# Kernel optimization log

Measured on AMD Instinct MI355X. Metric: run time of the kernel, lower is better.

The kernel has to match this reference:

```python
import jax, jax.numpy as jnp
import numpy as np

BN_EPS = 1e-5

def _sage_conv(x, src, dst, Wl, bl, Wr):
    # mean aggregation of neighbor messages: agg[v] = mean_{u->v} x[u]
    n = x.shape[0]
    s = jax.ops.segment_sum(x[src], dst, num_segments=n)            # [N, d]
    cnt = jax.ops.segment_sum(jnp.ones_like(dst, dtype=x.dtype), dst, num_segments=n)
    agg = s / jnp.maximum(cnt, 1.0)[:, None]
    return agg @ Wl + bl + x @ Wr                                   # lin_l(agg) + lin_r(x)

def _bn(x, g, b):
    mu = jnp.mean(x, axis=0)
    var = jnp.var(x, axis=0)
    return (x - mu) * jax.lax.rsqrt(var + BN_EPS) * g + b

def setup_inputs() -> dict:
    key = jax.random.key(0)
    ks = jax.random.split(key, 8)
    N, E, D, H, C = 100000, 1600000, 128, 128, 47
    sc = 1.0 / np.sqrt(D)
    return {
        "x": jax.random.normal(ks[0], (N, D), jnp.float32),
        "edge_index": jax.random.randint(ks[1], (2, E), 0, N, jnp.int64),
        "Wl0": jax.random.normal(ks[2], (D, H), jnp.float32) * sc,
        "bl0": jnp.zeros((H,), jnp.float32),
        "Wr0": jax.random.normal(ks[3], (D, H), jnp.float32) * sc,
        "g0": jnp.ones((H,), jnp.float32),
        "be0": jnp.zeros((H,), jnp.float32),
        "Wl1": jax.random.normal(ks[4], (H, H), jnp.float32) * sc,
        "bl1": jnp.zeros((H,), jnp.float32),
        "Wr1": jax.random.normal(ks[5], (H, H), jnp.float32) * sc,
        "g1": jnp.ones((H,), jnp.float32),
        "be1": jnp.zeros((H,), jnp.float32),
        "Wl2": jax.random.normal(ks[6], (H, C), jnp.float32) * sc,
        "bl2": jnp.zeros((C,), jnp.float32),
        "Wr2": jax.random.normal(ks[7], (H, C), jnp.float32) * sc,
    }

def reference(x, edge_index, Wl0, bl0, Wr0, g0, be0, Wl1, bl1, Wr1, g1, be1, Wl2, bl2, Wr2):
    src, dst = edge_index[0], edge_index[1]
    h = _sage_conv(x, src, dst, Wl0, bl0, Wr0)
    h = jax.nn.relu(_bn(h, g0, be0))
    h = _sage_conv(h, src, dst, Wl1, bl1, Wr1)
    h = jax.nn.relu(_bn(h, g1, be1))
    h = _sage_conv(h, src, dst, Wl2, bl2, Wr2)
    return jax.nn.log_softmax(h, axis=-1)
```

## Files before the change

### kernel.cpp

```cpp
#include <hip/hip_runtime.h>
#include <hip/hip_fp8.h>
#include <stdint.h>

#define AS1 __attribute__((address_space(1)))
#define AS3 __attribute__((address_space(3)))

typedef __bf16 bf16;
typedef __bf16 bf16x2 __attribute__((ext_vector_type(2)));
typedef __bf16 bf16x4v __attribute__((ext_vector_type(4)));
typedef __bf16 bf16x8 __attribute__((ext_vector_type(8)));
typedef float f32x4 __attribute__((ext_vector_type(4)));
typedef float f32x2 __attribute__((ext_vector_type(2)));
typedef __hip_fp8_e4m3 fp8;

#define BN_EPS 1e-5f
#define BKT_SHIFT 8
#define BKT_NODES 256
#define TILE_E 2048
#define NCOPY 16

__global__ void k_setup(const float* __restrict__ x, bf16* __restrict__ x_bf,
                        unsigned char* __restrict__ x8, int n4,
                        const int* __restrict__ ei, int* __restrict__ btot, int E, int nbkt,
                        const float* __restrict__ Wl0, const float* __restrict__ Wr0,
                        const float* __restrict__ Wl1, const float* __restrict__ Wr1,
                        const float* __restrict__ Wl2, const float* __restrict__ Wr2,
                        bf16* __restrict__ Bt0, bf16* __restrict__ Bt1, bf16* __restrict__ Bt2) {
    __shared__ int hist[512];
    const int tid = threadIdx.x;
    int g = blockIdx.x * 256 + tid;
    if (g < n4) {
        float4 v = ((const float4*)x)[g];
        bf16x4v o; o[0] = (bf16)v.x; o[1] = (bf16)v.y; o[2] = (bf16)v.z; o[3] = (bf16)v.w;
        ((bf16x4v*)x_bf)[g] = o;
        uchar4 o8;
        o8.x = fp8(v.x).__x; o8.y = fp8(v.y).__x; o8.z = fp8(v.z).__x; o8.w = fp8(v.w).__x;
        ((uchar4*)x8)[g] = o8;
    }
    if (blockIdx.x < 128) {
        int idx = g;
        int c = idx >> 8, k = idx & 255;
        float v0 = (k < 128) ? Wl0[k * 128 + c] : Wr0[(k - 128) * 128 + c];
        Bt0[c * 256 + k] = (bf16)v0;
        float v1 = (k < 128) ? Wl1[k * 128 + c] : Wr1[(k - 128) * 128 + c];
        Bt1[c * 256 + k] = (bf16)v1;
        if (k < 128) {
            float v2 = 0.f;
            if (c < 47)      v2 = Wl2[k * 47 + c];
            else if (c < 94) v2 = Wr2[k * 47 + (c - 47)];
            Bt2[c * 128 + k] = (bf16)v2;
        }
    }
    int nbinb = (E + 4095) / 4096;
    if (blockIdx.x < nbinb) {
        hist[tid] = 0; hist[tid + 256] = 0;
        __syncthreads();
        const int e0 = blockIdx.x * 4096;
        #pragma unroll
        for (int k = 0; k < 4; ++k) {
            int i4 = (e0 >> 2) + k * 256 + tid;
            if (i4 * 4 + 3 < E) {
                int4 d4 = ((const int4*)(ei + E))[i4];
                atomicAdd(&hist[d4.x >> BKT_SHIFT], 1);
                atomicAdd(&hist[d4.y >> BKT_SHIFT], 1);
                atomicAdd(&hist[d4.z >> BKT_SHIFT], 1);
                atomicAdd(&hist[d4.w >> BKT_SHIFT], 1);
            } else {
                for (int e = i4 * 4; e < min(E, i4 * 4 + 4); ++e)
                    atomicAdd(&hist[ei[E + e] >> BKT_SHIFT], 1);
            }
        }
        __syncthreads();
        for (int b = tid; b < nbkt; b += 256)
            if (hist[b]) atomicAdd(&btot[b], hist[b]);
    }
}

__device__ __forceinline__ void scan_btot(const int* __restrict__ btot, int nbkt,
                                          int* sb, int* wsum) {
    const int tid = threadIdx.x, lane = tid & 63, wid = tid >> 6;
    int a = (tid < nbkt) ? btot[tid] : 0;
    int b2 = (tid + 256 < nbkt) ? btot[tid + 256] : 0;
    int ia = a, ib = b2;
    #pragma unroll
    for (int d = 1; d < 64; d <<= 1) {
        int t1 = __shfl_up(ia, d, 64);
        int t2 = __shfl_up(ib, d, 64);
        if (lane >= d) { ia += t1; ib += t2; }
    }
    if (lane == 63) { wsum[wid] = ia; wsum[4 + wid] = ib; }
    __syncthreads();
    if (tid == 0) {
        int c = 0;
        #pragma unroll
        for (int i = 0; i < 8; ++i) { int t = wsum[i]; wsum[i] = c; c += t; }
    }
    __syncthreads();
    sb[tid] = ia - a + wsum[wid];
    sb[tid + 256] = ib - b2 + wsum[4 + wid];
    if (tid == 255) sb[512] = ib + wsum[7];
    __syncthreads();
}

__global__ __launch_bounds__(256) void k_bin(const int* __restrict__ ei,
                                             const int* __restrict__ btot,
                                             int* __restrict__ bfill,
                                             uint32_t* __restrict__ pair_buf,
                                             int E, int nbkt) {
    __shared__ int hist[512], gbase[512], hcur[512];
    __shared__ int sb[513], wsum[8];
    const int tid = threadIdx.x;
    const int e0 = blockIdx.x * TILE_E;
    hist[tid] = 0; hist[tid + 256] = 0;
    scan_btot(btot, nbkt, sb, wsum);

    int dreg[TILE_E / 256];
    #pragma unroll
    for (int k = 0; k < TILE_E / 256; ++k) {
        int e = e0 + k * 256 + tid;
        int d = (e < E) ? ei[E + e] : -1;
        dreg[k] = d;
        if (d >= 0) atomicAdd(&hist[d >> BKT_SHIFT], 1);
    }
    __syncthreads();

    for (int b = tid; b < nbkt; b += 256) {
        int h = hist[b];
        int g = (h > 0) ? atomicAdd(&bfill[b], h) : 0;
        gbase[b] = sb[b] + g;
        hcur[b] = 0;
    }
    __syncthreads();

    #pragma unroll
    for (int k = 0; k < TILE_E / 256; ++k) {
        int d = dreg[k];
        if (d >= 0) {
            int e = e0 + k * 256 + tid;
            int s = ei[e];
            int b = d >> BKT_SHIFT;
            int r = atomicAdd(&hcur[b], 1);
            pair_buf[(size_t)gbase[b] + r] =
                ((uint32_t)s << BKT_SHIFT) | (uint32_t)(d & (BKT_NODES - 1));
        }
    }
}

__global__ __launch_bounds__(256) void k_fill2(const uint32_t* __restrict__ pair_buf,
                                               const int* __restrict__ btot,
                                               int* __restrict__ row_ptr,
                                               float* __restrict__ inv_deg,
                                               int* __restrict__ col_idx,
                                               int n, int E, int nbkt) {
    __shared__ int hist[256], excl[256], hcur[256], wsum4[4];
    __shared__ int sb[513], wsum[8];
    const int b = blockIdx.x;
    const int tid = threadIdx.x, lane = tid & 63, wid = tid >> 6;
    const int n0 = b << BKT_SHIFT;
    hist[tid] = 0; hcur[tid] = 0;
    scan_btot(btot, nbkt, sb, wsum);
    const int s = sb[b], e = sb[b + 1];
    for (int i = s + tid; i < e; i += 256)
        atomicAdd(&hist[pair_buf[i] & (BKT_NODES - 1)], 1);
    __syncthreads();
    int v = hist[tid];
    int incl = v;
    #pragma unroll
    for (int d = 1; d < 64; d <<= 1) {
        int t = __shfl_up(incl, d, 64);
        if (lane >= d) incl += t;
    }
    if (lane == 63) wsum4[wid] = incl;
    __syncthreads();
    if (tid == 0) {
        int c = 0;
        #pragma unroll
        for (int i = 0; i < 4; ++i) { int t = wsum4[i]; wsum4[i] = c; c += t; }
    }
    __syncthreads();
    int ex = incl - v + wsum4[wid];
    excl[tid] = ex;
    int node = n0 + tid;
    if (node < n) {
        row_ptr[node] = s + ex;
        inv_deg[node] = 1.0f / (float)(v > 1 ? v : 1);
    }
    if (b == (int)gridDim.x - 1 && tid == 0) row_ptr[n] = E;
    __syncthreads();
    for (int i = s + tid; i < e; i += 256) {
        uint32_t pk = pair_buf[i];
        int dl = pk & (BKT_NODES - 1);
        int r = atomicAdd(&hcur[dl], 1);
        col_idx[s + excl[dl] + r] = (int)(pk >> BKT_SHIFT);
    }
}

#define ACC4(u) { f32x2 pl_ = __builtin_amdgcn_cvt_pk_f32_fp8(u, false); \
                  f32x2 ph_ = __builtin_amdgcn_cvt_pk_f32_fp8(u, true);  \
                  a0 += pl_[0]; a1 += pl_[1]; a2 += ph_[0]; a3 += ph_[1]; }
__global__ void k_aggregate(const unsigned char* __restrict__ src8, bf16* __restrict__ dst,
                            const int* __restrict__ row_ptr, const int* __restrict__ col_idx,
                            const float* __restrict__ inv_deg, int n) {
    const int lane = threadIdx.x & 63;
    const int half = lane >> 5;
    const int sl = lane & 31;
    const int node = blockIdx.x * 8 + ((threadIdx.x >> 6) << 1) + half;
    const bool valid = node < n;
    const int nn = valid ? node : 0;
    const int re0 = row_ptr[nn];
    const int re1 = valid ? row_ptr[nn + 1] : re0;
    const float inv = inv_deg[nn];
    const uint32_t l4 = (uint32_t)(sl << 2);
    float a0 = 0.f, a1 = 0.f, a2 = 0.f, a3 = 0.f;
    int e = re0;
    for (; e < re1 && (e & 3); ++e) {
        uint32_t u = *(const uint32_t*)(src8 + (((uint32_t)col_idx[e] << 7) + l4));
        ACC4(u)
    }
    for (; e + 16 <= re1; e += 16) {
        int4 i0 = *(const int4*)(col_idx + e);
        int4 i1 = *(const int4*)(col_idx + e + 4);
        int4 i2 = *(const int4*)(col_idx + e + 8);
        int4 i3 = *(const int4*)(col_idx + e + 12);
        uint32_t u0  = *(const uint32_t*)(src8 + (((uint32_t)i0.x << 7) + l4));
        uint32_t u1  = *(const uint32_t*)(src8 + (((uint32_t)i0.y << 7) + l4));
        uint32_t u2  = *(const uint32_t*)(src8 + (((uint32_t)i0.z << 7) + l4));
        uint32_t u3  = *(const uint32_t*)(src8 + (((uint32_t)i0.w << 7) + l4));
        uint32_t u4  = *(const uint32_t*)(src8 + (((uint32_t)i1.x << 7) + l4));
        uint32_t u5  = *(const uint32_t*)(src8 + (((uint32_t)i1.y << 7) + l4));
        uint32_t u6  = *(const uint32_t*)(src8 + (((uint32_t)i1.z << 7) + l4));
        uint32_t u7  = *(const uint32_t*)(src8 + (((uint32_t)i1.w << 7) + l4));
        uint32_t u8  = *(const uint32_t*)(src8 + (((uint32_t)i2.x << 7) + l4));
        uint32_t u9  = *(const uint32_t*)(src8 + (((uint32_t)i2.y << 7) + l4));
        uint32_t u10 = *(const uint32_t*)(src8 + (((uint32_t)i2.z << 7) + l4));
        uint32_t u11 = *(const uint32_t*)(src8 + (((uint32_t)i2.w << 7) + l4));
        uint32_t u12 = *(const uint32_t*)(src8 + (((uint32_t)i3.x << 7) + l4));
        uint32_t u13 = *(const uint32_t*)(src8 + (((uint32_t)i3.y << 7) + l4));
        uint32_t u14 = *(const uint32_t*)(src8 + (((uint32_t)i3.z << 7) + l4));
        uint32_t u15 = *(const uint32_t*)(src8 + (((uint32_t)i3.w << 7) + l4));
        ACC4(u0) ACC4(u1) ACC4(u2) ACC4(u3) ACC4(u4) ACC4(u5) ACC4(u6) ACC4(u7)
        ACC4(u8) ACC4(u9) ACC4(u10) ACC4(u11) ACC4(u12) ACC4(u13) ACC4(u14) ACC4(u15)
    }
    if (e < re1) {
        int4 i0 = *(const int4*)(col_idx + e);
        int4 i1 = *(const int4*)(col_idx + e + 4);
        int4 i2 = *(const int4*)(col_idx + e + 8);
        int4 i3 = *(const int4*)(col_idx + e + 12);
        bool k0  = e + 0  < re1, k1  = e + 1  < re1, k2  = e + 2  < re1, k3  = e + 3  < re1;
        bool k4  = e + 4  < re1, k5  = e + 5  < re1, k6  = e + 6  < re1, k7  = e + 7  < re1;
        bool k8  = e + 8  < re1, k9  = e + 9  < re1, k10 = e + 10 < re1, k11 = e + 11 < re1;
        bool k12 = e + 12 < re1, k13 = e + 13 < re1, k14 = e + 14 < re1, k15 = e + 15 < re1;
        int r0  = k0  ? i0.x : 0, r1  = k1  ? i0.y : 0, r2  = k2  ? i0.z : 0, r3  = k3  ? i0.w : 0;
        int r4  = k4  ? i1.x : 0, r5  = k5  ? i1.y : 0, r6  = k6  ? i1.z : 0, r7  = k7  ? i1.w : 0;
        int r8  = k8  ? i2.x : 0, r9  = k9  ? i2.y : 0, r10 = k10 ? i2.z : 0, r11 = k11 ? i2.w : 0;
        int r12 = k12 ? i3.x : 0, r13 = k13 ? i3.y : 0, r14 = k14 ? i3.z : 0, r15 = k15 ? i3.w : 0;
        uint32_t u0  = *(const uint32_t*)(src8 + (((uint32_t)r0  << 7) + l4));
        uint32_t u1  = *(const uint32_t*)(src8 + (((uint32_t)r1  << 7) + l4));
        uint32_t u2  = *(const uint32_t*)(src8 + (((uint32_t)r2  << 7) + l4));
        uint32_t u3  = *(const uint32_t*)(src8 + (((uint32_t)r3  << 7) + l4));
        uint32_t u4  = *(const uint32_t*)(src8 + (((uint32_t)r4  << 7) + l4));
        uint32_t u5  = *(const uint32_t*)(src8 + (((uint32_t)r5  << 7) + l4));
        uint32_t u6  = *(const uint32_t*)(src8 + (((uint32_t)r6  << 7) + l4));
        uint32_t u7  = *(const uint32_t*)(src8 + (((uint32_t)r7  << 7) + l4));
        uint32_t u8  = *(const uint32_t*)(src8 + (((uint32_t)r8  << 7) + l4));
        uint32_t u9  = *(const uint32_t*)(src8 + (((uint32_t)r9  << 7) + l4));
        uint32_t u10 = *(const uint32_t*)(src8 + (((uint32_t)r10 << 7) + l4));
        uint32_t u11 = *(const uint32_t*)(src8 + (((uint32_t)r11 << 7) + l4));
        uint32_t u12 = *(const uint32_t*)(src8 + (((uint32_t)r12 << 7) + l4));
        uint32_t u13 = *(const uint32_t*)(src8 + (((uint32_t)r13 << 7) + l4));
        uint32_t u14 = *(const uint32_t*)(src8 + (((uint32_t)r14 << 7) + l4));
        uint32_t u15 = *(const uint32_t*)(src8 + (((uint32_t)r15 << 7) + l4));
        u0  = k0  ? u0  : 0u; u1  = k1  ? u1  : 0u; u2  = k2  ? u2  : 0u; u3  = k3  ? u3  : 0u;
        u4  = k4  ? u4  : 0u; u5  = k5  ? u5  : 0u; u6  = k6  ? u6  : 0u; u7  = k7  ? u7  : 0u;
        u8  = k8  ? u8  : 0u; u9  = k9  ? u9  : 0u; u10 = k10 ? u10 : 0u; u11 = k11 ? u11 : 0u;
        u12 = k12 ? u12 : 0u; u13 = k13 ? u13 : 0u; u14 = k14 ? u14 : 0u; u15 = k15 ? u15 : 0u;
        ACC4(u0) ACC4(u1) ACC4(u2) ACC4(u3) ACC4(u4) ACC4(u5) ACC4(u6) ACC4(u7)
        ACC4(u8) ACC4(u9) ACC4(u10) ACC4(u11) ACC4(u12) ACC4(u13) ACC4(u14) ACC4(u15)
    }
    if (valid) {
        bf16x4v o;
        o[0] = (bf16)(a0 * inv); o[1] = (bf16)(a1 * inv);
        o[2] = (bf16)(a2 * inv); o[3] = (bf16)(a3 * inv);
        *(bf16x4v*)(dst + (size_t)node * 128 + (sl << 2)) = o;
    }
}
#undef ACC4

template<int CH, bool STATS, int NT>
__global__ __launch_bounds__(256) void k_gemm6(
    const bf16* __restrict__ A1, const bf16* __restrict__ A2, const bf16* __restrict__ Bt,
    const float* __restrict__ bias, bf16* __restrict__ outH,
    fp8* __restrict__ yl8, bf16* __restrict__ yrbf, float* __restrict__ stats, int M) {
    __shared__ __attribute__((aligned(16))) bf16 sA[2][4096];
    __shared__ __attribute__((aligned(16))) bf16 sB[2][4096];
    __shared__ float scol[128], scol2[128];
    constexpr int LDB = CH * 32;
    const int tid = threadIdx.x;
    const int w = tid >> 6, l = tid & 63;
    const int q = l >> 4, r = l & 15;
    const int r0 = blockIdx.x * 128;
    if (STATS && tid < 128) { scol[tid] = 0.f; scol2[tid] = 0.f; }

    auto stage = [&](int buf, int c) {
        const bf16* As = (c < 4) ? A1 : A2;
        const int ka = (c & 3) * 32;
        #pragma unroll
        for (int i = 0; i < 2; ++i) {
            const int T = w * 2 + i;
            const bf16* ga = As + (size_t)(r0 + T * 16 + r) * 128 + ka + q * 8;
            __builtin_amdgcn_global_load_lds((AS1 uint32_t*)(uintptr_t)ga,
                (AS3 uint32_t*)(uint32_t)(uintptr_t)(&sA[buf][T * 512]), 16, 0, 0);
            if (T < NT) {
                const bf16* gb = Bt + (T * 16 + r) * LDB + c * 32 + q * 8;
                __builtin_amdgcn_global_load_lds((AS1 uint32_t*)(uintptr_t)gb,
                    (AS3 uint32_t*)(uint32_t)(uintptr_t)(&sB[buf][T * 512]), 16, 0, 0);
            }
        }
    };

    f32x4 acc[2][NT];
    #pragma unroll
    for (int i = 0; i < 2; ++i)
        #pragma unroll
        for (int j = 0; j < NT; ++j) { acc[i][j][0] = 0.f; acc[i][j][1] = 0.f; acc[i][j][2] = 0.f; acc[i][j][3] = 0.f; }

    stage(0, 0);
    __syncthreads();

    #pragma unroll
    for (int c = 0; c < CH; ++c) {
        const int cur = c & 1;
        if (c + 1 < CH) stage(cur ^ 1, c + 1);
        bf16x8 af0 = *(const bf16x8*)&sA[cur][(w * 2 + 0) * 512 + q * 128 + r * 8];
        bf16x8 af1 = *(const bf16x8*)&sA[cur][(w * 2 + 1) * 512 + q * 128 + r * 8];
        #pragma unroll
        for (int ct = 0; ct < NT; ++ct) {
            bf16x8 bv = *(const bf16x8*)&sB[cur][ct * 512 + q * 128 + r * 8];
            acc[0][ct] = __builtin_amdgcn_mfma_f32_16x16x32_bf16(af0, bv, acc[0][ct], 0, 0, 0);
            acc[1][ct] = __builtin_amdgcn_mfma_f32_16x16x32_bf16(af1, bv, acc[1][ct], 0, 0, 0);
        }
        __syncthreads();
    }

    if (STATS) {
        #pragma unroll
        for (int ct = 0; ct < NT; ++ct) {
            int col = ct * 16 + r;
            float bv = bias ? bias[col] : 0.f;
            float s_c = 0.f, q_c = 0.f;
            #pragma unroll
            for (int rt = 0; rt < 2; ++rt) {
                #pragma unroll
                for (int j = 0; j < 4; ++j) {
                    int row = r0 + w * 32 + rt * 16 + q * 4 + j;
                    if (row < M) {
                        float v = acc[rt][ct][j] + bv;
                        outH[(size_t)row * 128 + col] = (bf16)v;
                        s_c += v; q_c += v * v;
                    }
                }
            }
            atomicAdd(&scol[col], s_c);
            atomicAdd(&scol2[col], q_c);
        }
        __syncthreads();
        float* sbase = stats + ((blockIdx.x & (NCOPY - 1)) << 8);
        if (tid < 128) {
            atomicAdd(&sbase[tid], scol[tid]);
            atomicAdd(&sbase[128 + tid], scol2[tid]);
        }
    } else {
        #pragma unroll
        for (int rt = 0; rt < 2; ++rt) {
            #pragma unroll
            for (int ct = 0; ct < NT; ++ct) {
                int col = ct * 16 + r;
                #pragma unroll
                for (int j = 0; j < 4; ++j) {
                    int row = r0 + w * 32 + rt * 16 + q * 4 + j;
                    if (row >= M) continue;
                    if (col < 47)      yl8[(size_t)row * 64 + col] = fp8(acc[rt][ct][j]);
                    else if (col < 94) yrbf[(size_t)row * 48 + (col - 47)] = (bf16)acc[rt][ct][j];
                }
            }
        }
    }
}

__global__ void k_bn_prep(const float* __restrict__ sums, const float* __restrict__ gma,
                          const float* __restrict__ bta, float* __restrict__ scsh, int n) {
    int col = threadIdx.x;
    float s = 0.f, q = 0.f;
    #pragma unroll
    for (int cpy = 0; cpy < NCOPY; ++cpy) {
        s += sums[(cpy << 8) + col];
        q += sums[(cpy << 8) + 128 + col];
    }
    float invn = 1.0f / (float)n;
    float mu = s * invn;
    float var = q * invn - mu * mu;
    float sc = gma[col] * rsqrtf(var + BN_EPS);
    scsh[col] = sc;
    scsh[128 + col] = bta[col] - mu * sc;
}

__global__ void k_bn_apply(const bf16* __restrict__ h, const float* __restrict__ scsh,
                           bf16* __restrict__ out, unsigned char* __restrict__ out8, int n) {
    int g = blockIdx.x * blockDim.x + threadIdx.x;
    int row = g >> 6, c2 = g & 63;
    if (row >= n) return;
    int col = c2 << 1;
    float2 sc = *(const float2*)(scsh + col);
    float2 sh = *(const float2*)(scsh + 128 + col);
    bf16x2 hv = *(const bf16x2*)(h + (size_t)row * 128 + col);
    float r0 = fmaxf((float)hv[0] * sc.x + sh.x, 0.f);
    float r1 = fmaxf((float)hv[1] * sc.y + sh.y, 0.f);
    bf16x2 o; o[0] = (bf16)r0; o[1] = (bf16)r1;
    *(bf16x2*)(out + (size_t)row * 128 + col) = o;
    uchar2 o8; o8.x = fp8(r0).__x; o8.y = fp8(r1).__x;
    *(uchar2*)(out8 + (size_t)row * 128 + col) = o8;
}

__global__ void k_final(const unsigned char* __restrict__ yl, const bf16* __restrict__ yr,
                        const int* __restrict__ row_ptr, const int* __restrict__ col_idx,
                        const float* __restrict__ inv_deg, const float* __restrict__ bl2,
                        float* __restrict__ out, int n) {
    int node = blockIdx.x * 4 + (threadIdx.x >> 6);
    int lane = threadIdx.x & 63;
    if (node >= n) return;
    int e0 = row_ptr[node], e1 = row_ptr[node + 1];
    float inv = inv_deg[node];
    const int sub = lane >> 4;
    const int c4 = lane & 15;
    const uint32_t loff = (uint32_t)(c4 << 2);
    float a0 = 0.f, a1 = 0.f, a2 = 0.f, a3 = 0.f;
    int base = e0;
    for (; base + 16 <= e1; base += 16) {
        int i0 = col_idx[base + sub];
        int i1 = col_idx[base + 4 + sub];
        int i2 = col_idx[base + 8 + sub];
        int i3 = col_idx[base + 12 + sub];
        uint32_t u0 = *(const uint32_t*)(yl + (((uint32_t)i0 << 6) + loff));
        uint32_t u1 = *(const uint32_t*)(yl + (((uint32_t)i1 << 6) + loff));
        uint32_t u2 = *(const uint32_t*)(yl + (((uint32_t)i2 << 6) + loff));
        uint32_t u3 = *(const uint32_t*)(yl + (((uint32_t)i3 << 6) + loff));
        f32x2 p0l = __builtin_amdgcn_cvt_pk_f32_fp8(u0, false);
        f32x2 p0h = __builtin_amdgcn_cvt_pk_f32_fp8(u0, true);
        f32x2 p1l = __builtin_amdgcn_cvt_pk_f32_fp8(u1, false);
        f32x2 p1h = __builtin_amdgcn_cvt_pk_f32_fp8(u1, true);
        f32x2 p2l = __builtin_amdgcn_cvt_pk_f32_fp8(u2, false);
        f32x2 p2h = __builtin_amdgcn_cvt_pk_f32_fp8(u2, true);
        f32x2 p3l = __builtin_amdgcn_cvt_pk_f32_fp8(u3, false);
        f32x2 p3h = __builtin_amdgcn_cvt_pk_f32_fp8(u3, true);
        a0 += (p0l[0] + p1l[0]) + (p2l[0] + p3l[0]);
        a1 += (p0l[1] + p1l[1]) + (p2l[1] + p3l[1]);
        a2 += (p0h[0] + p1h[0]) + (p2h[0] + p3h[0]);
        a3 += (p0h[1] + p1h[1]) + (p2h[1] + p3h[1]);
    }
    if (base < e1) {
        int ee0 = base + sub;
        int ee1 = base + 4 + sub;
        int ee2 = base + 8 + sub;
        int ee3 = base + 12 + sub;
        bool k0 = ee0 < e1, k1 = ee1 < e1, k2 = ee2 < e1, k3 = ee3 < e1;
        int i0 = col_idx[k0 ? ee0 : e0];
        int i1 = col_idx[k1 ? ee1 : e0];
        int i2 = col_idx[k2 ? ee2 : e0];
        int i3 = col_idx[k3 ? ee3 : e0];
        uint32_t u0 = *(const uint32_t*)(yl + (((uint32_t)i0 << 6) + loff));
        uint32_t u1 = *(const uint32_t*)(yl + (((uint32_t)i1 << 6) + loff));
        uint32_t u2 = *(const uint32_t*)(yl + (((uint32_t)i2 << 6) + loff));
        uint32_t u3 = *(const uint32_t*)(yl + (((uint32_t)i3 << 6) + loff));
        u0 = k0 ? u0 : 0u;
        u1 = k1 ? u1 : 0u;
        u2 = k2 ? u2 : 0u;
        u3 = k3 ? u3 : 0u;
        f32x2 p0l = __builtin_amdgcn_cvt_pk_f32_fp8(u0, false);
        f32x2 p0h = __builtin_amdgcn_cvt_pk_f32_fp8(u0, true);
        f32x2 p1l = __builtin_amdgcn_cvt_pk_f32_fp8(u1, false);
        f32x2 p1h = __builtin_amdgcn_cvt_pk_f32_fp8(u1, true);
        f32x2 p2l = __builtin_amdgcn_cvt_pk_f32_fp8(u2, false);
        f32x2 p2h = __builtin_amdgcn_cvt_pk_f32_fp8(u2, true);
        f32x2 p3l = __builtin_amdgcn_cvt_pk_f32_fp8(u3, false);
        f32x2 p3h = __builtin_amdgcn_cvt_pk_f32_fp8(u3, true);
        a0 += (p0l[0] + p1l[0]) + (p2l[0] + p3l[0]);
        a1 += (p0l[1] + p1l[1]) + (p2l[1] + p3l[1]);
        a2 += (p0h[0] + p1h[0]) + (p2h[0] + p3h[0]);
        a3 += (p0h[1] + p1h[1]) + (p2h[1] + p3h[1]);
    }
    a0 += __shfl_xor(a0, 16, 64); a1 += __shfl_xor(a1, 16, 64);
    a2 += __shfl_xor(a2, 16, 64); a3 += __shfl_xor(a3, 16, 64);
    a0 += __shfl_xor(a0, 32, 64); a1 += __shfl_xor(a1, 32, 64);
    a2 += __shfl_xor(a2, 32, 64); a3 += __shfl_xor(a3, 32, 64);
    const int f0 = c4 << 2;
    bf16x4v yv4 = *(const bf16x4v*)(yr + (size_t)node * 48 + f0);
    float v0 = (f0 + 0 < 47) ? fmaf(a0, inv, (float)yv4[0] + bl2[f0 + 0]) : -__builtin_inff();
    float v1 = (f0 + 1 < 47) ? fmaf(a1, inv, (float)yv4[1] + bl2[f0 + 1]) : -__builtin_inff();
    float v2 = (f0 + 2 < 47) ? fmaf(a2, inv, (float)yv4[2] + bl2[f0 + 2]) : -__builtin_inff();
    float v3 = (f0 + 3 < 47) ? fmaf(a3, inv, (float)yv4[3] + bl2[f0 + 3]) : -__builtin_inff();
    float m = fmaxf(fmaxf(v0, v1), fmaxf(v2, v3));
    #pragma unroll
    for (int o = 1; o < 16; o <<= 1) m = fmaxf(m, __shfl_xor(m, o, 64));
    float ex0 = (f0 + 0 < 47) ? __expf(v0 - m) : 0.f;
    float ex1 = (f0 + 1 < 47) ? __expf(v1 - m) : 0.f;
    float ex2 = (f0 + 2 < 47) ? __expf(v2 - m) : 0.f;
    float ex3 = (f0 + 3 < 47) ? __expf(v3 - m) : 0.f;
    float s = (ex0 + ex1) + (ex2 + ex3);
    #pragma unroll
    for (int o = 1; o < 16; o <<= 1) s += __shfl_xor(s, o, 64);
    float ls = __logf(s);
    if (lane < 16) {
        float* op = out + (size_t)node * 47 + f0;
        if (f0 + 0 < 47) op[0] = v0 - m - ls;
        if (f0 + 1 < 47) op[1] = v1 - m - ls;
        if (f0 + 2 < 47) op[2] = v2 - m - ls;
        if (f0 + 3 < 47) op[3] = v3 - m - ls;
    }
}

extern "C" void kernel_launch(void* const* d_in, const int* in_sizes, int n_in,
                              void* d_out, int out_size, void* d_ws, size_t ws_size,
                              hipStream_t stream) {
    const float* x   = (const float*)d_in[0];
    const int*   ei  = (const int*)d_in[1];
    const float* Wl0 = (const float*)d_in[2];
    const float* bl0 = (const float*)d_in[3];
    const float* Wr0 = (const float*)d_in[4];
    const float* g0  = (const float*)d_in[5];
    const float* be0 = (const float*)d_in[6];
    const float* Wl1 = (const float*)d_in[7];
    const float* bl1 = (const float*)d_in[8];
    const float* Wr1 = (const float*)d_in[9];
    const float* g1  = (const float*)d_in[10];
    const float* be1 = (const float*)d_in[11];
    const float* Wl2 = (const float*)d_in[12];
    const float* bl2 = (const float*)d_in[13];
    const float* Wr2 = (const float*)d_in[14];
    float* out = (float*)d_out;

    const int N  = in_sizes[0] / 128;
    const int E  = in_sizes[1] / 2;
    const int NP = ((N + 127) / 128) * 128;
    const int NBKT = (N + BKT_NODES - 1) / BKT_NODES;

    char* p = (char*)d_ws;
    size_t off = 0;
    auto alloc = [&](size_t b) { char* r = p + off; off += (b + 255) & ~(size_t)255; return r; };
    int*   bfill   = (int*)alloc(1024 * 4);
    float* bnsum   = (float*)alloc(2 * NCOPY * 256 * 4);
    int*   btot    = (int*)alloc(512 * 4);
    size_t zero_span = off;
    float* scsh    = (float*)alloc(2 * 256 * 4);
    int*   row_ptr = (int*)alloc((size_t)(N + 1) * 4);
    float* invd    = (float*)alloc((size_t)N * 4);
    int*   col_idx = (int*)alloc((size_t)E * 4);
    uint32_t* pair_buf = (uint32_t*)alloc((size_t)E * 4);
    bf16*  x_bf    = (bf16*)alloc((size_t)NP * 128 * 2);
    bf16*  aggbf   = (bf16*)alloc((size_t)NP * 128 * 2);
    bf16*  hbf     = (bf16*)alloc((size_t)NP * 128 * 2);
    unsigned char* h8 = (unsigned char*)alloc((size_t)NP * 128);
    float* bufF    = (float*)alloc((size_t)NP * 128 * 4 + 256);
    bf16*  Bt0     = (bf16*)alloc(128 * 256 * 2);
    bf16*  Bt1     = (bf16*)alloc(128 * 256 * 2);
    bf16*  Bt2     = (bf16*)alloc(128 * 128 * 2);
    unsigned char* x8 = (unsigned char*)bufF;
    bf16*  hraw = (bf16*)bufF;
    fp8*   yl8  = (fp8*)bufF;
    bf16*  yrbf = (bf16*)((char*)bufF + (size_t)NP * 64);

    hipMemsetAsync(bfill, 0, zero_span, stream);

    int n4 = N * 128 / 4;
    k_setup<<<(n4 + 255) / 256, 256, 0, stream>>>(x, x_bf, x8, n4, ei, btot, E, NBKT,
                                                  Wl0, Wr0, Wl1, Wr1, Wl2, Wr2, Bt0, Bt1, Bt2);
    k_bin<<<(E + TILE_E - 1) / TILE_E, 256, 0, stream>>>(ei, btot, bfill, pair_buf, E, NBKT);
    k_fill2<<<NBKT, 256, 0, stream>>>(pair_buf, btot, row_ptr, invd, col_idx, N, E, NBKT);

    int aggBlocks  = (N + 7) / 8;
    int gemmBlocks = NP / 128;
    int bnBlocks   = (N * 64 + 255) / 256;
    int finBlocks  = (N + 3) / 4;

    k_aggregate<<<aggBlocks, 256, 0, stream>>>(x8, aggbf, row_ptr, col_idx, invd, N);
    k_gemm6<8, true, 8><<<gemmBlocks, 256, 0, stream>>>(aggbf, x_bf, Bt0, bl0, hraw, nullptr, nullptr, bnsum, N);
    k_bn_prep<<<1, 128, 0, stream>>>(bnsum, g0, be0, scsh, N);
    k_bn_apply<<<bnBlocks, 256, 0, stream>>>(hraw, scsh, hbf, h8, N);
    k_aggregate<<<aggBlocks, 256, 0, stream>>>(h8, aggbf, row_ptr, col_idx, invd, N);
    k_gemm6<8, true, 8><<<gemmBlocks, 256, 0, stream>>>(aggbf, hbf, Bt1, bl1, hraw, nullptr, nullptr, bnsum + NCOPY * 256, N);
    k_bn_prep<<<1, 128, 0, stream>>>(bnsum + NCOPY * 256, g1, be1, scsh + 256, N);
    k_bn_apply<<<bnBlocks, 256, 0, stream>>>(hraw, scsh + 256, hbf, h8, N);
    k_gemm6<4, false, 6><<<gemmBlocks, 256, 0, stream>>>(hbf, hbf, Bt2, nullptr, nullptr, yl8, yrbf, nullptr, N);
    k_final<<<finBlocks, 256, 0, stream>>>((const unsigned char*)yl8, yrbf, row_ptr, col_idx, invd, bl2, out, N);
}
```

Measured before the change: 453.3 us.

## Load A fragments directly from global and preload full B into LDS

The GEMM kernel no longer stages A tiles through LDS with double buffering. Each wave now reads its A fragments straight from global memory into registers. The whole weight matrix B is loaded into LDS once up front, which removes the per-chunk __syncthreads barriers. This cuts LDS traffic and synchronisation, but A loads are now exposed global latency with no explicit prefetch. LDS use grows to CH*NT*512 bf16 (64KB for CH=8, NT=8), which may reduce occupancy.

```diff
diff --git a/kernel.cpp b/kernel.cpp
--- a/kernel.cpp
+++ b/kernel.cpp
@@ -287,12 +287,11 @@
 #undef ACC4
 
 template<int CH, bool STATS, int NT>
-__global__ __launch_bounds__(256) void k_gemm6(
+__global__ __launch_bounds__(256) void k_gemm7(
     const bf16* __restrict__ A1, const bf16* __restrict__ A2, const bf16* __restrict__ Bt,
     const float* __restrict__ bias, bf16* __restrict__ outH,
     fp8* __restrict__ yl8, bf16* __restrict__ yrbf, float* __restrict__ stats, int M) {
-    __shared__ __attribute__((aligned(16))) bf16 sA[2][4096];
-    __shared__ __attribute__((aligned(16))) bf16 sB[2][4096];
+    __shared__ __attribute__((aligned(16))) bf16 sB[CH * NT * 512];
     __shared__ float scol[128], scol2[128];
     constexpr int LDB = CH * 32;
     const int tid = threadIdx.x;
@@ -301,22 +300,24 @@
     const int r0 = blockIdx.x * 128;
     if (STATS && tid < 128) { scol[tid] = 0.f; scol2[tid] = 0.f; }
 
-    auto stage = [&](int buf, int c) {
-        const bf16* As = (c < 4) ? A1 : A2;
-        const int ka = (c & 3) * 32;
+    #pragma unroll
+    for (int c = 0; c < CH; ++c) {
         #pragma unroll
         for (int i = 0; i < 2; ++i) {
             const int T = w * 2 + i;
-            const bf16* ga = As + (size_t)(r0 + T * 16 + r) * 128 + ka + q * 8;
-            __builtin_amdgcn_global_load_lds((AS1 uint32_t*)(uintptr_t)ga,
-                (AS3 uint32_t*)(uint32_t)(uintptr_t)(&sA[buf][T * 512]), 16, 0, 0);
             if (T < NT) {
                 const bf16* gb = Bt + (T * 16 + r) * LDB + c * 32 + q * 8;
                 __builtin_amdgcn_global_load_lds((AS1 uint32_t*)(uintptr_t)gb,
-                    (AS3 uint32_t*)(uint32_t)(uintptr_t)(&sB[buf][T * 512]), 16, 0, 0);
+                    (AS3 uint32_t*)(uint32_t)(uintptr_t)(&sB[(c * NT + T) * 512]), 16, 0, 0);
             }
         }
-    };
+    }
+
+    const uint32_t aoff = ((uint32_t)(r0 + w * 32 + r) << 7) + (uint32_t)(q << 3);
+    const bf16* pa0_1 = A1 + aoff;
+    const bf16* pa1_1 = A1 + aoff + 16 * 128;
+    const bf16* pa0_2 = A2 + aoff;
+    const bf16* pa1_2 = A2 + aoff + 16 * 128;
 
     f32x4 acc[2][NT];
     #pragma unroll
@@ -324,22 +325,21 @@
         #pragma unroll
         for (int j = 0; j < NT; ++j) { acc[i][j][0] = 0.f; acc[i][j][1] = 0.f; acc[i][j][2] = 0.f; acc[i][j][3] = 0.f; }
 
-    stage(0, 0);
     __syncthreads();
 
     #pragma unroll
     for (int c = 0; c < CH; ++c) {
-        const int cur = c & 1;
-        if (c + 1 < CH) stage(cur ^ 1, c + 1);
-        bf16x8 af0 = *(const bf16x8*)&sA[cur][(w * 2 + 0) * 512 + q * 128 + r * 8];
-        bf16x8 af1 = *(const bf16x8*)&sA[cur][(w * 2 + 1) * 512 + q * 128 + r * 8];
+        const bf16* p0 = (c < 4) ? pa0_1 : pa0_2;
+        const bf16* p1 = (c < 4) ? pa1_1 : pa1_2;
+        const int ka = (c & 3) * 32;
+        bf16x8 af0 = *(const bf16x8*)(p0 + ka);
+        bf16x8 af1 = *(const bf16x8*)(p1 + ka);
         #pragma unroll
         for (int ct = 0; ct < NT; ++ct) {
-            bf16x8 bv = *(const bf16x8*)&sB[cur][ct * 512 + q * 128 + r * 8];
+            bf16x8 bv = *(const bf16x8*)&sB[(c * NT + ct) * 512 + q * 128 + r * 8];
             acc[0][ct] = __builtin_amdgcn_mfma_f32_16x16x32_bf16(af0, bv, acc[0][ct], 0, 0, 0);
             acc[1][ct] = __builtin_amdgcn_mfma_f32_16x16x32_bf16(af1, bv, acc[1][ct], 0, 0, 0);
         }
-        __syncthreads();
     }
 
     if (STATS) {
@@ -582,13 +582,13 @@
     int finBlocks  = (N + 3) / 4;
 
     k_aggregate<<<aggBlocks, 256, 0, stream>>>(x8, aggbf, row_ptr, col_idx, invd, N);
-    k_gemm6<8, true, 8><<<gemmBlocks, 256, 0, stream>>>(aggbf, x_bf, Bt0, bl0, hraw, nullptr, nullptr, bnsum, N);
+    k_gemm7<8, true, 8><<<gemmBlocks, 256, 0, stream>>>(aggbf, x_bf, Bt0, bl0, hraw, nullptr, nullptr, bnsum, N);
     k_bn_prep<<<1, 128, 0, stream>>>(bnsum, g0, be0, scsh, N);
     k_bn_apply<<<bnBlocks, 256, 0, stream>>>(hraw, scsh, hbf, h8, N);
     k_aggregate<<<aggBlocks, 256, 0, stream>>>(h8, aggbf, row_ptr, col_idx, invd, N);
-    k_gemm6<8, true, 8><<<gemmBlocks, 256, 0, stream>>>(aggbf, hbf, Bt1, bl1, hraw, nullptr, nullptr, bnsum + NCOPY * 256, N);
+    k_gemm7<8, true, 8><<<gemmBlocks, 256, 0, stream>>>(aggbf, hbf, Bt1, bl1, hraw, nullptr, nullptr, bnsum + NCOPY * 256, N);
     k_bn_prep<<<1, 128, 0, stream>>>(bnsum + NCOPY * 256, g1, be1, scsh + 256, N);
     k_bn_apply<<<bnBlocks, 256, 0, stream>>>(hraw, scsh + 256, hbf, h8, N);
-    k_gemm6<4, false, 6><<<gemmBlocks, 256, 0, stream>>>(hbf, hbf, Bt2, nullptr, nullptr, yl8, yrbf, nullptr, N);
+    k_gemm7<4, false, 6><<<gemmBlocks, 256, 0, stream>>>(hbf, hbf, Bt2, nullptr, nullptr, yl8, yrbf, nullptr, N);
     k_final<<<finBlocks, 256, 0, stream>>>((const unsigned char*)yl8, yrbf, row_ptr, col_idx, invd, bl2, out, N);
 }
```

Measured after the change: 444.3 us. 1.02x faster.
